# Kernel tuning notes

Measured on AMD Instinct MI355X. Metric: run time of the kernel, lower is better.

## Reference

```python
import jax, jax.numpy as jnp
import numpy as np

B, S, E, A = 8, 127, 512, 256  # batch, seq (pre-sentinel), encoder dim, arc representation dim

_BRANCHES = ["sib_head", "sib_dep", "cop_head", "cop_dep", "gp_head", "gp_dep", "gp_head_dep"]


def setup_inputs() -> dict:
    key = jax.random.key(0)
    ks = jax.random.split(key, 16)
    d = {
        "x": jax.random.normal(ks[0], (B, S, E), jnp.float32),
        "pos_tags": jax.random.randint(ks[1], (B, S), 0, 48),
        "mask": jnp.ones((B, S), jnp.int32),
    }
    for i, n in enumerate(_BRANCHES):
        d[f"W_{n}"] = jax.random.normal(ks[2 + i], (E, A), jnp.float32) * (1.0 / np.sqrt(E))
        d[f"b_{n}"] = jnp.zeros((A,), jnp.float32)
    for i, n in enumerate(["sib", "cop", "gp"]):
        d[f"U_{n}"] = jax.random.normal(ks[9 + i], (A, A, A), jnp.float32) * (1.0 / A)
    d["sentinel"] = jax.random.normal(ks[12], (E,), jnp.float32)
    return d


def _tri(u, v, w, U):
    # trilinear (triaffine) score: s[b,i,j,k] = sum_{a,c,d} u[b,i,a] U[a,c,d] v[b,j,c] w[b,k,d]
    t = jnp.einsum('bia,acd->bicd', u, U)       # [B, n, A, A]
    t = jnp.einsum('bicd,bjc->bijd', t, v)      # [B, n, n, A]
    return jnp.einsum('bijd,bkd->bijk', t, w)   # [B, n, n, n]


def reference(x, pos_tags, mask,
              W_sib_head, b_sib_head, W_sib_dep, b_sib_dep,
              W_cop_head, b_cop_head, W_cop_dep, b_cop_dep,
              W_gp_head, b_gp_head, W_gp_dep, b_gp_dep,
              W_gp_head_dep, b_gp_head_dep,
              U_sib, U_cop, U_gp, sentinel):
    b, _, e = x.shape
    # prepend head sentinel token
    h = jnp.concatenate([jnp.broadcast_to(sentinel, (b, 1, e)), x], axis=1)  # [B, n, E]
    mask_full = jnp.concatenate([jnp.ones((b, 1), mask.dtype), mask], axis=1)
    elu = jax.nn.elu
    sib_head = elu(h @ W_sib_head + b_sib_head)
    sib_dep = elu(h @ W_sib_dep + b_sib_dep)
    cop_head = elu(h @ W_cop_head + b_cop_head)
    cop_dep = elu(h @ W_cop_dep + b_cop_dep)
    gp_head = elu(h @ W_gp_head + b_gp_head)
    gp_dep = elu(h @ W_gp_dep + b_gp_dep)
    gp_head_dep = elu(h @ W_gp_head_dep + b_gp_head_dep)
    sib = _tri(sib_head, sib_dep, sib_dep, U_sib)
    cop = _tri(cop_head, cop_dep, cop_head, U_cop)
    gp = _tri(gp_head, gp_head_dep, gp_dep, U_gp)
    return sib, cop, gp, mask_full
```

## Files before the change

### kernel.cpp

```cpp
#include <hip/hip_runtime.h>
#include <math.h>

#define N_TOK 128
#define ADIM  256
#define EDIM  512
#define BSZ   8
#define NSQ   65536
#define PAD   40

typedef short bf16x8 __attribute__((ext_vector_type(8)));
typedef float f32x4  __attribute__((ext_vector_type(4)));
#define MFMA_BF16(a, b, c) __builtin_amdgcn_mfma_f32_16x16x32_bf16((a), (b), (c), 0, 0, 0)

__device__ inline short f2bf(float f) {
  union { float f; unsigned u; } v; v.f = f;
  unsigned r = v.u + 0x7fff + ((v.u >> 16) & 1);
  return (short)(r >> 16);
}

struct ProjArgs {
  const float* W[7];
  const float* b[7];
};

__global__ __launch_bounds__(256) void proj_kernel(
    const float* __restrict__ x, const float* __restrict__ sentinel,
    ProjArgs args, short* __restrict__ proj)
{
  const int p  = blockIdx.y;
  const int m0 = blockIdx.x * 8;
  const int tid = threadIdx.x;
  __shared__ float hs[8][EDIM];
  #pragma unroll
  for (int q = 0; q < 16; ++q) {
    int idx = tid + q * 256;
    int r = idx >> 9, c = idx & 511;
    int m = m0 + r, b = m >> 7, i = m & 127;
    hs[r][c] = (i == 0) ? sentinel[c] : x[((size_t)(b * 127) + (i - 1)) * EDIM + c];
  }
  __syncthreads();
  const float* W = args.W[p];
  float bias = args.b[p][tid];
  float acc[8];
  #pragma unroll
  for (int r = 0; r < 8; ++r) acc[r] = bias;
  #pragma unroll 4
  for (int k = 0; k < EDIM; ++k) {
    float wv = W[(size_t)k * ADIM + tid];
    #pragma unroll
    for (int r = 0; r < 8; ++r) acc[r] = fmaf(hs[r][k], wv, acc[r]);
  }
  short* outp = proj + ((size_t)p * (BSZ * N_TOK) + m0) * ADIM + tid;
  #pragma unroll
  for (int r = 0; r < 8; ++r) {
    float v = acc[r];
    v = v > 0.f ? v : expm1f(v);
    outp[(size_t)r * ADIM] = f2bf(v);
  }
}

__global__ __launch_bounds__(256) void permU(
    const float* __restrict__ U, short* __restrict__ Ut)
{
  __shared__ float tile[64][69];
  const int c  = blockIdx.x;
  const int a0 = blockIdx.y * 64;
  const int d0 = blockIdx.z * 64;
  const int t  = threadIdx.x;
  {
    int ar = t >> 4, ds4 = (t & 15) * 4;
    #pragma unroll
    for (int q = 0; q < 4; ++q) {
      int a = ar + q * 16;
      float4 v = *(const float4*)&U[(size_t)(a0 + a) * NSQ + c * 256 + d0 + ds4];
      tile[a][ds4] = v.x; tile[a][ds4 + 1] = v.y;
      tile[a][ds4 + 2] = v.z; tile[a][ds4 + 3] = v.w;
    }
  }
  __syncthreads();
  {
    int dr = t >> 4, as4 = (t & 15) * 4;
    #pragma unroll
    for (int q = 0; q < 4; ++q) {
      int d = dr + q * 16;
      ushort4 o;
      o.x = (unsigned short)f2bf(tile[as4 + 0][d]);
      o.y = (unsigned short)f2bf(tile[as4 + 1][d]);
      o.z = (unsigned short)f2bf(tile[as4 + 2][d]);
      o.w = (unsigned short)f2bf(tile[as4 + 3][d]);
      *(ushort4*)&Ut[((size_t)(d0 + d) * 256 + c) * 256 + a0 + as4] = o;
    }
  }
}

__global__ __launch_bounds__(256) void gemm_t1(
    const short* __restrict__ A,
    const short* __restrict__ Ut,
    short* __restrict__ C)
{
  __shared__ short As[128][PAD];
  __shared__ short Bs[128][PAD];
  const int tid = threadIdx.x;
  const int wave = tid >> 6, lane = tid & 63;
  const int ln15 = lane & 15, quad = lane >> 4;
  const int m0 = blockIdx.x * 128, n0 = blockIdx.y * 128;
  const int wm = (wave & 1) * 64, wn = (wave >> 1) * 64;
  f32x4 acc[4][4] = {};
  for (int kt = 0; kt < ADIM; kt += 32) {
    __syncthreads();
    #pragma unroll
    for (int p = 0; p < 2; ++p) {
      int q = tid + p * 256;
      int r = q >> 2, s = q & 3;
      *(uint4*)&As[r][s * 8] = *(const uint4*)&A [(size_t)(m0 + r) * ADIM + kt + s * 8];
      *(uint4*)&Bs[r][s * 8] = *(const uint4*)&Ut[(size_t)(n0 + r) * ADIM + kt + s * 8];
    }
    __syncthreads();
    bf16x8 af[4], bfr[4];
    #pragma unroll
    for (int r = 0; r < 4; ++r)  af[r]  = *(bf16x8*)&As[wm + r * 16 + ln15][quad * 8];
    #pragma unroll
    for (int c2 = 0; c2 < 4; ++c2) bfr[c2] = *(bf16x8*)&Bs[wn + c2 * 16 + ln15][quad * 8];
    #pragma unroll
    for (int r = 0; r < 4; ++r)
      #pragma unroll
      for (int c2 = 0; c2 < 4; ++c2)
        acc[r][c2] = MFMA_BF16(af[r], bfr[c2], acc[r][c2]);
  }
  #pragma unroll
  for (int r = 0; r < 4; ++r)
    #pragma unroll
    for (int c2 = 0; c2 < 4; ++c2)
      #pragma unroll
      for (int e = 0; e < 4; ++e) {
        int m = m0 + wm + r * 16 + quad * 4 + e;
        int n = n0 + wn + c2 * 16 + ln15;
        C[(size_t)m * NSQ + n] = f2bf(acc[r][c2][e]);
      }
}

__global__ __launch_bounds__(256) void fuse_mfma(
    const short* __restrict__ t1,
    const short* __restrict__ projv,
    const short* __restrict__ projw,
    float* __restrict__ out,
    int b0)
{
  __shared__ short Bs[256][PAD];
  __shared__ short Avs[64][PAD];
  __shared__ short Ws[128][PAD];
  __shared__ short t2s[64][264];
  const int i  = blockIdx.x;
  const int bl = blockIdx.y;
  const int b  = b0 + bl;
  const int tid = threadIdx.x;
  const int wave = tid >> 6, lane = tid & 63;
  const int ln15 = lane & 15, quad = lane >> 4;
  const short* t1row = t1 + (size_t)(bl * N_TOK + i) * NSQ;
  const size_t vb = (size_t)b * N_TOK * ADIM;
  const size_t wb = (size_t)b * N_TOK * ADIM;
  float* obase = out + (size_t)(b * N_TOK + i) * N_TOK * N_TOK;

  for (int jh = 0; jh < 2; ++jh) {
    const int wj = (wave & 1) * 32, wd = (wave >> 1) * 128;
    f32x4 acc[2][8] = {};
    for (int ct = 0; ct < ADIM; ct += 32) {
      __syncthreads();
      #pragma unroll
      for (int p = 0; p < 4; ++p) {
        int q = tid + p * 256;
        int r = q >> 2, s = q & 3;
        *(uint4*)&Bs[r][s * 8] = *(const uint4*)&t1row[(size_t)r * ADIM + ct + s * 8];
      }
      {
        int r = tid >> 2, s = tid & 3;
        *(uint4*)&Avs[r][s * 8] =
            *(const uint4*)&projv[vb + (size_t)(jh * 64 + r) * ADIM + ct + s * 8];
      }
      __syncthreads();
      bf16x8 af[2];
      #pragma unroll
      for (int fr = 0; fr < 2; ++fr)
        af[fr] = *(bf16x8*)&Avs[wj + fr * 16 + ln15][quad * 8];
      #pragma unroll
      for (int fc = 0; fc < 8; ++fc) {
        bf16x8 bfc = *(bf16x8*)&Bs[wd + fc * 16 + ln15][quad * 8];
        #pragma unroll
        for (int fr = 0; fr < 2; ++fr)
          acc[fr][fc] = MFMA_BF16(af[fr], bfc, acc[fr][fc]);
      }
    }
    __syncthreads();
    #pragma unroll
    for (int fr = 0; fr < 2; ++fr)
      #pragma unroll
      for (int fc = 0; fc < 8; ++fc)
        #pragma unroll
        for (int e = 0; e < 4; ++e)
          t2s[wj + fr * 16 + quad * 4 + e][wd + fc * 16 + ln15] = f2bf(acc[fr][fc][e]);
    __syncthreads();

    const int wj2 = (wave & 1) * 32, wk = (wave >> 1) * 64;
    f32x4 acc2[2][4] = {};
    for (int dt = 0; dt < ADIM; dt += 32) {
      __syncthreads();
      #pragma unroll
      for (int p = 0; p < 2; ++p) {
        int q = tid + p * 256;
        int r = q >> 2, s = q & 3;
        *(uint4*)&Ws[r][s * 8] =
            *(const uint4*)&projw[wb + (size_t)r * ADIM + dt + s * 8];
      }
      __syncthreads();
      bf16x8 a2[2], b2[4];
      #pragma unroll
      for (int fr = 0; fr < 2; ++fr)
        a2[fr] = *(bf16x8*)&t2s[wj2 + fr * 16 + ln15][dt + quad * 8];
      #pragma unroll
      for (int fc = 0; fc < 4; ++fc)
        b2[fc] = *(bf16x8*)&Ws[wk + fc * 16 + ln15][quad * 8];
      #pragma unroll
      for (int fr = 0; fr < 2; ++fr)
        #pragma unroll
        for (int fc = 0; fc < 4; ++fc)
          acc2[fr][fc] = MFMA_BF16(a2[fr], b2[fc], acc2[fr][fc]);
    }
    #pragma unroll
    for (int fr = 0; fr < 2; ++fr)
      #pragma unroll
      for (int fc = 0; fc < 4; ++fc)
        #pragma unroll
        for (int e = 0; e < 4; ++e) {
          int j  = jh * 64 + wj2 + fr * 16 + quad * 4 + e;
          int k2 = wk + fc * 16 + ln15;
          obase[(size_t)j * N_TOK + k2] = acc2[fr][fc][e];
        }
  }
}

__global__ void mask_kernel(const int* __restrict__ mask, float* __restrict__ out) {
  int idx = blockIdx.x * 256 + threadIdx.x;
  if (idx < BSZ * N_TOK) {
    int b = idx >> 7, i = idx & 127;
    out[idx] = (i == 0) ? 1.0f : (float)mask[b * 127 + i - 1];
  }
}

extern "C" void kernel_launch(void* const* d_in, const int* in_sizes, int n_in,
                              void* d_out, int out_size, void* d_ws, size_t ws_size,
                              hipStream_t stream)
{
  const float* x    = (const float*)d_in[0];
  const int*   mask = (const int*)d_in[2];
  ProjArgs pa;
  for (int p = 0; p < 7; ++p) {
    pa.W[p] = (const float*)d_in[3 + 2 * p];
    pa.b[p] = (const float*)d_in[4 + 2 * p];
  }
  const float* Us[3] = {(const float*)d_in[17], (const float*)d_in[18],
                        (const float*)d_in[19]};
  const float* sentinel = (const float*)d_in[20];

  short* proj = (short*)d_ws;
  const size_t ut_off  = 4u << 20;
  const size_t t1_off  = ut_off + ((size_t)NSQ * ADIM * 2);
  short* Ut = (short*)((char*)d_ws + ut_off);
  short* t1 = (short*)((char*)d_ws + t1_off);
  size_t avail = (ws_size > t1_off) ? ws_size - t1_off : 0;
  int cb = 8;
  while (cb > 1 && (size_t)cb * N_TOK * NSQ * 2 > avail) cb >>= 1;

  proj_kernel<<<dim3(128, 7), 256, 0, stream>>>(x, sentinel, pa, proj);

  const int u_idx[3] = {0, 2, 4};
  const int v_idx[3] = {1, 3, 6};
  const int w_idx[3] = {1, 2, 5};
  float* outp = (float*)d_out;

  for (int sc = 0; sc < 3; ++sc) {
    permU<<<dim3(256, 4, 4), 256, 0, stream>>>(Us[sc], Ut);
    for (int b0 = 0; b0 < BSZ; b0 += cb) {
      const short* A = proj + ((size_t)u_idx[sc] * 1024 + (size_t)b0 * N_TOK) * ADIM;
      gemm_t1<<<dim3(cb, 512), 256, 0, stream>>>(A, Ut, t1);
      fuse_mfma<<<dim3(128, cb), 256, 0, stream>>>(
          t1,
          proj + (size_t)v_idx[sc] * 1024 * ADIM,
          proj + (size_t)w_idx[sc] * 1024 * ADIM,
          outp + (size_t)sc * BSZ * N_TOK * N_TOK * N_TOK,
          b0);
    }
  }
  mask_kernel<<<dim3(4), 256, 0, stream>>>(
      mask, outp + (size_t)3 * BSZ * N_TOK * N_TOK * N_TOK);
}
```

Before: 931.7 us.

## Split fused t2/score kernel into two separate 128x128 MFMA GEMM kernels

Replaces the fused per-row kernel, which computed the t2 intermediate in shared memory and then the scores, with two standalone GEMM kernels. The new kernels use 128x128 tiles with 4x4 MFMA fragments per wave, and t2 goes through a global workspace buffer in bf16. This is meant to raise MFMA utilisation and occupancy, since the fused kernel used small tiles and a large shared-memory footprint. In exchange it adds a global write and read of t2 (B*128*128*256 bf16 per branch), more workspace, and an extra kernel launch per chunk.

```diff
diff --git a/kernel.cpp b/kernel.cpp
--- a/kernel.cpp
+++ b/kernel.cpp
@@ -139,103 +139,110 @@
       }
 }
 
-__global__ __launch_bounds__(256) void fuse_mfma(
+__global__ __launch_bounds__(256) void gemm_t2(
     const short* __restrict__ t1,
     const short* __restrict__ projv,
+    short* __restrict__ t2,
+    int b0)
+{
+  __shared__ short As[128][PAD];
+  __shared__ short Bs[128][PAD];
+  const int tid = threadIdx.x;
+  const int wave = tid >> 6, lane = tid & 63;
+  const int ln15 = lane & 15, quad = lane >> 4;
+  const int n0 = blockIdx.x * 128;
+  const int bl = blockIdx.y;
+  const int b  = b0 + bl;
+  const short* Bt = t1 + (size_t)bl * N_TOK * NSQ;
+  const short* Av = projv + (size_t)b * N_TOK * ADIM;
+  const int wm = (wave & 1) * 64, wn = (wave >> 1) * 64;
+  f32x4 acc[4][4] = {};
+  for (int kt = 0; kt < ADIM; kt += 32) {
+    __syncthreads();
+    #pragma unroll
+    for (int p = 0; p < 2; ++p) {
+      int q = tid + p * 256;
+      int r = q >> 2, s = q & 3;
+      *(uint4*)&As[r][s * 8] = *(const uint4*)&Av[(size_t)r * ADIM + kt + s * 8];
+      *(uint4*)&Bs[r][s * 8] = *(const uint4*)&Bt[(size_t)(n0 + r) * ADIM + kt + s * 8];
+    }
+    __syncthreads();
+    bf16x8 af[4], bfr[4];
+    #pragma unroll
+    for (int r = 0; r < 4; ++r)  af[r]  = *(bf16x8*)&As[wm + r * 16 + ln15][quad * 8];
+    #pragma unroll
+    for (int c2 = 0; c2 < 4; ++c2) bfr[c2] = *(bf16x8*)&Bs[wn + c2 * 16 + ln15][quad * 8];
+    #pragma unroll
+    for (int r = 0; r < 4; ++r)
+      #pragma unroll
+      for (int c2 = 0; c2 < 4; ++c2)
+        acc[r][c2] = MFMA_BF16(af[r], bfr[c2], acc[r][c2]);
+  }
+  const int i     = n0 >> 8;
+  const int dbase = n0 & 255;
+  short* ob = t2 + (size_t)bl * (N_TOK * N_TOK * ADIM) + (size_t)i * (N_TOK * ADIM);
+  #pragma unroll
+  for (int r = 0; r < 4; ++r)
+    #pragma unroll
+    for (int c2 = 0; c2 < 4; ++c2)
+      #pragma unroll
+      for (int e = 0; e < 4; ++e) {
+        int j = wm + r * 16 + quad * 4 + e;
+        int d = dbase + wn + c2 * 16 + ln15;
+        ob[(size_t)j * ADIM + d] = f2bf(acc[r][c2][e]);
+      }
+}
+
+__global__ __launch_bounds__(256) void gemm_s(
+    const short* __restrict__ t2,
     const short* __restrict__ projw,
     float* __restrict__ out,
     int b0)
 {
-  __shared__ short Bs[256][PAD];
-  __shared__ short Avs[64][PAD];
-  __shared__ short Ws[128][PAD];
-  __shared__ short t2s[64][264];
-  const int i  = blockIdx.x;
-  const int bl = blockIdx.y;
-  const int b  = b0 + bl;
+  __shared__ short As[128][PAD];
+  __shared__ short Bs[128][PAD];
   const int tid = threadIdx.x;
   const int wave = tid >> 6, lane = tid & 63;
   const int ln15 = lane & 15, quad = lane >> 4;
-  const short* t1row = t1 + (size_t)(bl * N_TOK + i) * NSQ;
-  const size_t vb = (size_t)b * N_TOK * ADIM;
-  const size_t wb = (size_t)b * N_TOK * ADIM;
-  float* obase = out + (size_t)(b * N_TOK + i) * N_TOK * N_TOK;
-
-  for (int jh = 0; jh < 2; ++jh) {
-    const int wj = (wave & 1) * 32, wd = (wave >> 1) * 128;
-    f32x4 acc[2][8] = {};
-    for (int ct = 0; ct < ADIM; ct += 32) {
-      __syncthreads();
-      #pragma unroll
-      for (int p = 0; p < 4; ++p) {
-        int q = tid + p * 256;
-        int r = q >> 2, s = q & 3;
-        *(uint4*)&Bs[r][s * 8] = *(const uint4*)&t1row[(size_t)r * ADIM + ct + s * 8];
+  const int m0 = blockIdx.x * 128;
+  const int bl = blockIdx.y;
+  const int b  = b0 + bl;
+  const short* At = t2 + (size_t)bl * (N_TOK * N_TOK * ADIM);
+  const short* Bw = projw + (size_t)b * N_TOK * ADIM;
+  float* ob = out + (size_t)b * N_TOK * N_TOK * N_TOK + (size_t)m0 * N_TOK;
+  const int wm = (wave & 1) * 64, wn = (wave >> 1) * 64;
+  f32x4 acc[4][4] = {};
+  for (int kt = 0; kt < ADIM; kt += 32) {
+    __syncthreads();
+    #pragma unroll
+    for (int p = 0; p < 2; ++p) {
+      int q = tid + p * 256;
+      int r = q >> 2, s = q & 3;
+      *(uint4*)&As[r][s * 8] = *(const uint4*)&At[(size_t)(m0 + r) * ADIM + kt + s * 8];
+      *(uint4*)&Bs[r][s * 8] = *(const uint4*)&Bw[(size_t)r * ADIM + kt + s * 8];
+    }
+    __syncthreads();
+    bf16x8 af[4], bfr[4];
+    #pragma unroll
+    for (int r = 0; r < 4; ++r)  af[r]  = *(bf16x8*)&As[wm + r * 16 + ln15][quad * 8];
+    #pragma unroll
+    for (int c2 = 0; c2 < 4; ++c2) bfr[c2] = *(bf16x8*)&Bs[wn + c2 * 16 + ln15][quad * 8];
+    #pragma unroll
+    for (int r = 0; r < 4; ++r)
+      #pragma unroll
+      for (int c2 = 0; c2 < 4; ++c2)
+        acc[r][c2] = MFMA_BF16(af[r], bfr[c2], acc[r][c2]);
+  }
+  #pragma unroll
+  for (int r = 0; r < 4; ++r)
+    #pragma unroll
+    for (int c2 = 0; c2 < 4; ++c2)
+      #pragma unroll
+      for (int e = 0; e < 4; ++e) {
+        int m = wm + r * 16 + quad * 4 + e;
+        int k = wn + c2 * 16 + ln15;
+        ob[(size_t)m * N_TOK + k] = acc[r][c2][e];
       }
-      {
-        int r = tid >> 2, s = tid & 3;
-        *(uint4*)&Avs[r][s * 8] =
-            *(const uint4*)&projv[vb + (size_t)(jh * 64 + r) * ADIM + ct + s * 8];
-      }
-      __syncthreads();
-      bf16x8 af[2];
-      #pragma unroll
-      for (int fr = 0; fr < 2; ++fr)
-        af[fr] = *(bf16x8*)&Avs[wj + fr * 16 + ln15][quad * 8];
-      #pragma unroll
-      for (int fc = 0; fc < 8; ++fc) {
-        bf16x8 bfc = *(bf16x8*)&Bs[wd + fc * 16 + ln15][quad * 8];
-        #pragma unroll
-        for (int fr = 0; fr < 2; ++fr)
-          acc[fr][fc] = MFMA_BF16(af[fr], bfc, acc[fr][fc]);
-      }
-    }
-    __syncthreads();
-    #pragma unroll
-    for (int fr = 0; fr < 2; ++fr)
-      #pragma unroll
-      for (int fc = 0; fc < 8; ++fc)
-        #pragma unroll
-        for (int e = 0; e < 4; ++e)
-          t2s[wj + fr * 16 + quad * 4 + e][wd + fc * 16 + ln15] = f2bf(acc[fr][fc][e]);
-    __syncthreads();
-
-    const int wj2 = (wave & 1) * 32, wk = (wave >> 1) * 64;
-    f32x4 acc2[2][4] = {};
-    for (int dt = 0; dt < ADIM; dt += 32) {
-      __syncthreads();
-      #pragma unroll
-      for (int p = 0; p < 2; ++p) {
-        int q = tid + p * 256;
-        int r = q >> 2, s = q & 3;
-        *(uint4*)&Ws[r][s * 8] =
-            *(const uint4*)&projw[wb + (size_t)r * ADIM + dt + s * 8];
-      }
-      __syncthreads();
-      bf16x8 a2[2], b2[4];
-      #pragma unroll
-      for (int fr = 0; fr < 2; ++fr)
-        a2[fr] = *(bf16x8*)&t2s[wj2 + fr * 16 + ln15][dt + quad * 8];
-      #pragma unroll
-      for (int fc = 0; fc < 4; ++fc)
-        b2[fc] = *(bf16x8*)&Ws[wk + fc * 16 + ln15][quad * 8];
-      #pragma unroll
-      for (int fr = 0; fr < 2; ++fr)
-        #pragma unroll
-        for (int fc = 0; fc < 4; ++fc)
-          acc2[fr][fc] = MFMA_BF16(a2[fr], b2[fc], acc2[fr][fc]);
-    }
-    #pragma unroll
-    for (int fr = 0; fr < 2; ++fr)
-      #pragma unroll
-      for (int fc = 0; fc < 4; ++fc)
-        #pragma unroll
-        for (int e = 0; e < 4; ++e) {
-          int j  = jh * 64 + wj2 + fr * 16 + quad * 4 + e;
-          int k2 = wk + fc * 16 + ln15;
-          obase[(size_t)j * N_TOK + k2] = acc2[fr][fc][e];
-        }
-  }
 }
 
 __global__ void mask_kernel(const int* __restrict__ mask, float* __restrict__ out) {
@@ -262,13 +269,16 @@
   const float* sentinel = (const float*)d_in[20];
 
   short* proj = (short*)d_ws;
-  const size_t ut_off  = 4u << 20;
-  const size_t t1_off  = ut_off + ((size_t)NSQ * ADIM * 2);
+  const size_t ut_off = 4u << 20;
+  const size_t t1_off = ut_off + ((size_t)NSQ * ADIM * 2);
   short* Ut = (short*)((char*)d_ws + ut_off);
+  size_t avail = (ws_size > t1_off) ? ws_size - t1_off : 0;
+  const size_t t1_chunk = (size_t)N_TOK * NSQ * 2;
+  const size_t t2_chunk = (size_t)N_TOK * N_TOK * ADIM * 2;
+  int cb = 8;
+  while (cb > 1 && (size_t)cb * (t1_chunk + t2_chunk) > avail) cb >>= 1;
   short* t1 = (short*)((char*)d_ws + t1_off);
-  size_t avail = (ws_size > t1_off) ? ws_size - t1_off : 0;
-  int cb = 8;
-  while (cb > 1 && (size_t)cb * N_TOK * NSQ * 2 > avail) cb >>= 1;
+  short* t2 = (short*)((char*)d_ws + t1_off + (size_t)cb * t1_chunk);
 
   proj_kernel<<<dim3(128, 7), 256, 0, stream>>>(x, sentinel, pa, proj);
 
@@ -282,12 +292,11 @@
     for (int b0 = 0; b0 < BSZ; b0 += cb) {
       const short* A = proj + ((size_t)u_idx[sc] * 1024 + (size_t)b0 * N_TOK) * ADIM;
       gemm_t1<<<dim3(cb, 512), 256, 0, stream>>>(A, Ut, t1);
-      fuse_mfma<<<dim3(128, cb), 256, 0, stream>>>(
-          t1,
-          proj + (size_t)v_idx[sc] * 1024 * ADIM,
-          proj + (size_t)w_idx[sc] * 1024 * ADIM,
-          outp + (size_t)sc * BSZ * N_TOK * N_TOK * N_TOK,
-          b0);
+      gemm_t2<<<dim3(256, cb), 256, 0, stream>>>(
+          t1, proj + (size_t)v_idx[sc] * 1024 * ADIM, t2, b0);
+      gemm_s<<<dim3(128, cb), 256, 0, stream>>>(
+          t2, proj + (size_t)w_idx[sc] * 1024 * ADIM,
+          outp + (size_t)sc * BSZ * N_TOK * N_TOK * N_TOK, b0);
     }
   }
   mask_kernel<<<dim3(4), 256, 0, stream>>>(
```

Result: faster. 898.3 us (-3.6%).
